# Performance work log

Hardware: AMD Instinct MI355X
Metric: run time of the kernel (lower is better)

Reference implementation:

```python
import jax, jax.numpy as jnp
import numpy as np

# Per-field vocab sizes for the 17 sorted cat fields (ClientID large, ProductID=top1000+UNK)
VOCAB = np.array([500, 50, 100, 3, 1000000, 10, 20, 100, 2, 2, 1001, 4, 4, 50, 2000, 10, 7], dtype=np.int64)
OFFSETS = jnp.asarray(np.concatenate([[0], np.cumsum(VOCAB[:-1])]).astype(np.int32))  # [17]
TOTAL_VOCAB = int(VOCAB.sum())
EMBED_DIM = 16
N_NUM = 23
B = 262144


def setup_inputs() -> dict:
    key = jax.random.key(0)
    k1, k2, k3, k4 = jax.random.split(key, 4)
    # raw randints, folded into each field's valid range
    raw = jax.random.randint(k1, (B, 17), 0, 1000000, dtype=jnp.int32)
    x_cat = raw % jnp.asarray(VOCAB.astype(np.int32))  # [B,17], in-range per field
    x_num = jax.random.normal(k2, (B, N_NUM), dtype=jnp.float32)
    # all 17 per-field embedding tables concatenated into one big table
    table = jax.random.normal(k3, (TOTAL_VOCAB, EMBED_DIM), dtype=jnp.float32) * 0.01
    W_num = jax.random.normal(k4, (EMBED_DIM, N_NUM), dtype=jnp.float32) * 0.1  # Linear(23,16,bias=False) weight
    bias = jnp.zeros((1,), dtype=jnp.float32)  # global_bias
    return {"x_cat": x_cat, "x_num": x_num, "table": table, "W_num": W_num, "bias": bias}


def reference(x_cat, x_num, table, W_num, bias):
    # Fused gather of all 17 field embeddings: E[b,f,:] = embeddings[field_f](x_cat[b,f])
    E = table[x_cat + OFFSETS[None, :]]            # [B,17,16]
    s = E.sum(axis=1)                               # sum of field embeddings, [B,16]
    emb_num = x_num @ W_num.T                       # [B,16]
    # linear_part.sum() in the original
    linear = (s + emb_num).sum(axis=-1)             # [B]
    # sum_{i<j} (e_i . e_j) via 0.5*((sum e)^2 - sum e^2) identity (same math as the double loop)
    inter = 0.5 * ((s * s).sum(axis=-1) - (E * E).sum(axis=(1, 2)))  # [B]
    return bias[0] + linear + inter                 # [B] logits (batched version of scalar logit)
```

## Files before the change

kernel.cpp:

```cpp
#include <hip/hip_runtime.h>

#define NF 17
#define NN 23
#define ED 16
#define BLK 1024
#define RPP 256
#define RPB 512
#define SROWS 862
#define SSTR 20

typedef int   int4u   __attribute__((ext_vector_type(4), aligned(4)));
typedef float float4u __attribute__((ext_vector_type(4), aligned(4)));
typedef float float2u __attribute__((ext_vector_type(2), aligned(4)));

__device__ __forceinline__ void acc4(const float4 v, float& s0, float& s1,
                                     float& s2, float& s3, float& sq) {
    s0 += v.x; s1 += v.y; s2 += v.z; s3 += v.w;
    sq += v.x * v.x + v.y * v.y + v.z * v.z + v.w * v.w;
}

__global__ __launch_bounds__(BLK, 4) void ffm_fwd_kernel(
    const int* __restrict__ x_cat,
    const float* __restrict__ x_num,
    const float* __restrict__ table,
    const float* __restrict__ W_num,
    const float* __restrict__ bias,
    float* __restrict__ out,
    int nrows)
{
    __shared__ float tab[SROWS * SSTR];
    __shared__ float wsum[24];

    const int tid = threadIdx.x;
    const int rl  = tid >> 2;
    const int g   = tid & 3;
    const int wb  = 6 * g;

    const int row0 = blockIdx.x * RPB + rl;
    const int row1 = row0 + RPP;
    const int r0c = (row0 < nrows) ? row0 : (nrows - 1);
    const int r1c = (row1 < nrows) ? row1 : (nrows - 1);

    const int* xc0 = x_cat + (size_t)r0c * NF;
    int4u a0 = *(const int4u*)(xc0);
    int4u a1 = *(const int4u*)(xc0 + 4);
    int4u a2 = *(const int4u*)(xc0 + 8);
    int4u a3 = *(const int4u*)(xc0 + 12);
    int  a16 = xc0[16];
    const float* xp0 = x_num + (size_t)r0c * NN;
    float4u xa0 = *(const float4u*)(xp0 + wb);
    float xb0_0, xb1_0;
    if (g < 3) { const float2u t = *(const float2u*)(xp0 + wb + 4); xb0_0 = t.x; xb1_0 = t.y; }
    else       { xb0_0 = xp0[22]; xb1_0 = 0.f; }

    if (tid < 24) {
        float a = 0.f;
        if (tid < NN) {
            #pragma unroll
            for (int d = 0; d < ED; ++d) a += W_num[d * NN + tid];
        }
        wsum[tid] = a;
    }

    for (int i = tid; i < SROWS * 4; i += BLK) {
        const int r = i >> 2, q = i & 3;
        const int d = (r < 653) ? 0 : (r < 787) ? 1000000 : (r < 845) ? 1001001 : 1003001;
        *(float4*)&tab[r * SSTR + q * 4] =
            *(const float4*)(table + (size_t)(r + d) * ED + q * 4);
    }
    __syncthreads();

    const float b0 = bias[0];
    const float w0 = wsum[wb],     w1 = wsum[wb + 1], w2 = wsum[wb + 2],
                w3 = wsum[wb + 3], w4 = wsum[wb + 4], w5 = wsum[wb + 5];

    const float4 gv00 = *(const float4*)(table + (size_t)(a1.x +     653) * ED + g * 4);
    const float4 gv01 = *(const float4*)(table + (size_t)(a2.z + 1000787) * ED + g * 4);
    const float4 gv02 = *(const float4*)(table + (size_t)(a3.z + 1001846) * ED + g * 4);

    const int* xc1 = x_cat + (size_t)r1c * NF;
    int4u b0v = *(const int4u*)(xc1);
    int4u b1v = *(const int4u*)(xc1 + 4);
    int4u b2v = *(const int4u*)(xc1 + 8);
    int4u b3v = *(const int4u*)(xc1 + 12);
    int  b16v = xc1[16];
    const float* xp1 = x_num + (size_t)r1c * NN;
    float4u xa1 = *(const float4u*)(xp1 + wb);
    float xb0_1, xb1_1;
    if (g < 3) { const float2u t = *(const float2u*)(xp1 + wb + 4); xb0_1 = t.x; xb1_1 = t.y; }
    else       { xb0_1 = xp1[22]; xb1_1 = 0.f; }

    {
        float lin = xa0.x * w0 + xa0.y * w1 + xa0.z * w2 + xa0.w * w3
                  + xb0_0 * w4 + xb1_0 * w5;
        int pr[14];
        pr[0]  = a0.x;        pr[1]  = 500 + a0.y;  pr[2]  = 550 + a0.z;
        pr[3]  = 650 + a0.w;  pr[4]  = 653 + a1.y;  pr[5]  = 663 + a1.z;
        pr[6]  = 683 + a1.w;  pr[7]  = 783 + a2.x;  pr[8]  = 785 + a2.y;
        pr[9]  = 787 + a2.w;  pr[10] = 791 + a3.x;  pr[11] = 795 + a3.y;
        pr[12] = 845 + a3.w;  pr[13] = 855 + a16;

        float s0 = 0.f, s1 = 0.f, s2 = 0.f, s3 = 0.f, sq = 0.f;
        #pragma unroll
        for (int k = 0; k < 14; ++k)
            acc4(*(const float4*)&tab[pr[k] * SSTR + g * 4], s0, s1, s2, s3, sq);

        acc4(gv00, s0, s1, s2, s3, sq);
        acc4(gv01, s0, s1, s2, s3, sq);
        acc4(gv02, s0, s1, s2, s3, sq);

        float ssum = s0 + s1 + s2 + s3;
        float ss2  = s0 * s0 + s1 * s1 + s2 * s2 + s3 * s3;
        #pragma unroll
        for (int m = 1; m <= 2; m <<= 1) {
            ssum += __shfl_xor(ssum, m);
            ss2  += __shfl_xor(ss2, m);
            sq   += __shfl_xor(sq, m);
            lin  += __shfl_xor(lin, m);
        }
        if (g == 0 && row0 < nrows) out[row0] = b0 + ssum + lin + 0.5f * (ss2 - sq);
    }

    const float4 gv10 = *(const float4*)(table + (size_t)(b1v.x +     653) * ED + g * 4);
    const float4 gv11 = *(const float4*)(table + (size_t)(b2v.z + 1000787) * ED + g * 4);
    const float4 gv12 = *(const float4*)(table + (size_t)(b3v.z + 1001846) * ED + g * 4);

    {
        float lin = xa1.x * w0 + xa1.y * w1 + xa1.z * w2 + xa1.w * w3
                  + xb0_1 * w4 + xb1_1 * w5;
        int pr[14];
        pr[0]  = b0v.x;        pr[1]  = 500 + b0v.y;  pr[2]  = 550 + b0v.z;
        pr[3]  = 650 + b0v.w;  pr[4]  = 653 + b1v.y;  pr[5]  = 663 + b1v.z;
        pr[6]  = 683 + b1v.w;  pr[7]  = 783 + b2v.x;  pr[8]  = 785 + b2v.y;
        pr[9]  = 787 + b2v.w;  pr[10] = 791 + b3v.x;  pr[11] = 795 + b3v.y;
        pr[12] = 845 + b3v.w;  pr[13] = 855 + b16v;

        float s0 = 0.f, s1 = 0.f, s2 = 0.f, s3 = 0.f, sq = 0.f;
        #pragma unroll
        for (int k = 0; k < 14; ++k)
            acc4(*(const float4*)&tab[pr[k] * SSTR + g * 4], s0, s1, s2, s3, sq);

        acc4(gv10, s0, s1, s2, s3, sq);
        acc4(gv11, s0, s1, s2, s3, sq);
        acc4(gv12, s0, s1, s2, s3, sq);

        float ssum = s0 + s1 + s2 + s3;
        float ss2  = s0 * s0 + s1 * s1 + s2 * s2 + s3 * s3;
        #pragma unroll
        for (int m = 1; m <= 2; m <<= 1) {
            ssum += __shfl_xor(ssum, m);
            ss2  += __shfl_xor(ss2, m);
            sq   += __shfl_xor(sq, m);
            lin  += __shfl_xor(lin, m);
        }
        if (g == 0 && row1 < nrows) out[row1] = b0 + ssum + lin + 0.5f * (ss2 - sq);
    }
}

extern "C" void kernel_launch(void* const* d_in, const int* in_sizes, int n_in,
                              void* d_out, int out_size, void* d_ws, size_t ws_size,
                              hipStream_t stream) {
    const int*   x_cat = (const int*)  d_in[0];
    const float* x_num = (const float*)d_in[1];
    const float* table = (const float*)d_in[2];
    const float* W_num = (const float*)d_in[3];
    const float* bias  = (const float*)d_in[4];
    float* out = (float*)d_out;

    const int nrows = out_size;
    const int grid = (nrows + RPB - 1) / RPB;
    ffm_fwd_kernel<<<grid, BLK, 0, stream>>>(x_cat, x_num, table, W_num, bias, out, nrows);
}
```

Measured before the change: 21.47 us.

## Issue big-table gathers early, merge shuffle reductions, drop row bounds checks

```diff
diff --git a/kernel.cpp b/kernel.cpp
--- a/kernel.cpp
+++ b/kernel.cpp
@@ -19,7 +19,7 @@
     sq += v.x * v.x + v.y * v.y + v.z * v.z + v.w * v.w;
 }
 
-__global__ __launch_bounds__(BLK, 4) void ffm_fwd_kernel(
+__global__ __launch_bounds__(BLK, 8) void ffm_fwd_kernel(
     const int* __restrict__ x_cat,
     const float* __restrict__ x_num,
     const float* __restrict__ table,
@@ -38,17 +38,19 @@
 
     const int row0 = blockIdx.x * RPB + rl;
     const int row1 = row0 + RPP;
-    const int r0c = (row0 < nrows) ? row0 : (nrows - 1);
-    const int r1c = (row1 < nrows) ? row1 : (nrows - 1);
 
-    const int* xc0 = x_cat + (size_t)r0c * NF;
-    int4u a0 = *(const int4u*)(xc0);
-    int4u a1 = *(const int4u*)(xc0 + 4);
-    int4u a2 = *(const int4u*)(xc0 + 8);
-    int4u a3 = *(const int4u*)(xc0 + 12);
-    int  a16 = xc0[16];
-    const float* xp0 = x_num + (size_t)r0c * NN;
-    float4u xa0 = *(const float4u*)(xp0 + wb);
+    const int* xc0 = x_cat + (size_t)row0 * NF;
+    const int4u a0 = *(const int4u*)(xc0);
+    const int4u a1 = *(const int4u*)(xc0 + 4);
+    const int4u a2 = *(const int4u*)(xc0 + 8);
+    const int4u a3 = *(const int4u*)(xc0 + 12);
+    const int  a16 = xc0[16];
+    const float4 gv00 = *(const float4*)(table + (size_t)(a1.x +     653) * ED + g * 4);
+    const float4 gv01 = *(const float4*)(table + (size_t)(a2.z + 1000787) * ED + g * 4);
+    const float4 gv02 = *(const float4*)(table + (size_t)(a3.z + 1001846) * ED + g * 4);
+
+    const float* xp0 = x_num + (size_t)row0 * NN;
+    const float4u xa0 = *(const float4u*)(xp0 + wb);
     float xb0_0, xb1_0;
     if (g < 3) { const float2u t = *(const float2u*)(xp0 + wb + 4); xb0_0 = t.x; xb1_0 = t.y; }
     else       { xb0_0 = xp0[22]; xb1_0 = 0.f; }
@@ -74,21 +76,12 @@
     const float w0 = wsum[wb],     w1 = wsum[wb + 1], w2 = wsum[wb + 2],
                 w3 = wsum[wb + 3], w4 = wsum[wb + 4], w5 = wsum[wb + 5];
 
-    const float4 gv00 = *(const float4*)(table + (size_t)(a1.x +     653) * ED + g * 4);
-    const float4 gv01 = *(const float4*)(table + (size_t)(a2.z + 1000787) * ED + g * 4);
-    const float4 gv02 = *(const float4*)(table + (size_t)(a3.z + 1001846) * ED + g * 4);
-
-    const int* xc1 = x_cat + (size_t)r1c * NF;
-    int4u b0v = *(const int4u*)(xc1);
-    int4u b1v = *(const int4u*)(xc1 + 4);
-    int4u b2v = *(const int4u*)(xc1 + 8);
-    int4u b3v = *(const int4u*)(xc1 + 12);
-    int  b16v = xc1[16];
-    const float* xp1 = x_num + (size_t)r1c * NN;
-    float4u xa1 = *(const float4u*)(xp1 + wb);
-    float xb0_1, xb1_1;
-    if (g < 3) { const float2u t = *(const float2u*)(xp1 + wb + 4); xb0_1 = t.x; xb1_1 = t.y; }
-    else       { xb0_1 = xp1[22]; xb1_1 = 0.f; }
+    const int* xc1 = x_cat + (size_t)row1 * NF;
+    const int4u c0 = *(const int4u*)(xc1);
+    const int4u c1 = *(const int4u*)(xc1 + 4);
+    const int4u c2 = *(const int4u*)(xc1 + 8);
+    const int4u c3 = *(const int4u*)(xc1 + 12);
+    const int  c16 = xc1[16];
 
     {
         float lin = xa0.x * w0 + xa0.y * w1 + xa0.z * w2 + xa0.w * w3
@@ -109,31 +102,32 @@
         acc4(gv01, s0, s1, s2, s3, sq);
         acc4(gv02, s0, s1, s2, s3, sq);
 
-        float ssum = s0 + s1 + s2 + s3;
-        float ss2  = s0 * s0 + s1 * s1 + s2 * s2 + s3 * s3;
-        #pragma unroll
-        for (int m = 1; m <= 2; m <<= 1) {
-            ssum += __shfl_xor(ssum, m);
-            ss2  += __shfl_xor(ss2, m);
-            sq   += __shfl_xor(sq, m);
-            lin  += __shfl_xor(lin, m);
-        }
-        if (g == 0 && row0 < nrows) out[row0] = b0 + ssum + lin + 0.5f * (ss2 - sq);
+        float contrib = (s0 + s1 + s2 + s3) + lin
+                      + 0.5f * ((s0 * s0 + s1 * s1 + s2 * s2 + s3 * s3) - sq);
+        contrib += __shfl_xor(contrib, 1);
+        contrib += __shfl_xor(contrib, 2);
+        if (g == 0) out[row0] = b0 + contrib;
     }
 
-    const float4 gv10 = *(const float4*)(table + (size_t)(b1v.x +     653) * ED + g * 4);
-    const float4 gv11 = *(const float4*)(table + (size_t)(b2v.z + 1000787) * ED + g * 4);
-    const float4 gv12 = *(const float4*)(table + (size_t)(b3v.z + 1001846) * ED + g * 4);
+    const float4 gv10 = *(const float4*)(table + (size_t)(c1.x +     653) * ED + g * 4);
+    const float4 gv11 = *(const float4*)(table + (size_t)(c2.z + 1000787) * ED + g * 4);
+    const float4 gv12 = *(const float4*)(table + (size_t)(c3.z + 1001846) * ED + g * 4);
+
+    const float* xp1 = x_num + (size_t)row1 * NN;
+    const float4u xa1 = *(const float4u*)(xp1 + wb);
+    float xb0_1, xb1_1;
+    if (g < 3) { const float2u t = *(const float2u*)(xp1 + wb + 4); xb0_1 = t.x; xb1_1 = t.y; }
+    else       { xb0_1 = xp1[22]; xb1_1 = 0.f; }
 
     {
         float lin = xa1.x * w0 + xa1.y * w1 + xa1.z * w2 + xa1.w * w3
                   + xb0_1 * w4 + xb1_1 * w5;
         int pr[14];
-        pr[0]  = b0v.x;        pr[1]  = 500 + b0v.y;  pr[2]  = 550 + b0v.z;
-        pr[3]  = 650 + b0v.w;  pr[4]  = 653 + b1v.y;  pr[5]  = 663 + b1v.z;
-        pr[6]  = 683 + b1v.w;  pr[7]  = 783 + b2v.x;  pr[8]  = 785 + b2v.y;
-        pr[9]  = 787 + b2v.w;  pr[10] = 791 + b3v.x;  pr[11] = 795 + b3v.y;
-        pr[12] = 845 + b3v.w;  pr[13] = 855 + b16v;
+        pr[0]  = c0.x;        pr[1]  = 500 + c0.y;  pr[2]  = 550 + c0.z;
+        pr[3]  = 650 + c0.w;  pr[4]  = 653 + c1.y;  pr[5]  = 663 + c1.z;
+        pr[6]  = 683 + c1.w;  pr[7]  = 783 + c2.x;  pr[8]  = 785 + c2.y;
+        pr[9]  = 787 + c2.w;  pr[10] = 791 + c3.x;  pr[11] = 795 + c3.y;
+        pr[12] = 845 + c3.w;  pr[13] = 855 + c16;
 
         float s0 = 0.f, s1 = 0.f, s2 = 0.f, s3 = 0.f, sq = 0.f;
         #pragma unroll
@@ -144,16 +138,11 @@
         acc4(gv11, s0, s1, s2, s3, sq);
         acc4(gv12, s0, s1, s2, s3, sq);
 
-        float ssum = s0 + s1 + s2 + s3;
-        float ss2  = s0 * s0 + s1 * s1 + s2 * s2 + s3 * s3;
-        #pragma unroll
-        for (int m = 1; m <= 2; m <<= 1) {
-            ssum += __shfl_xor(ssum, m);
-            ss2  += __shfl_xor(ss2, m);
-            sq   += __shfl_xor(sq, m);
-            lin  += __shfl_xor(lin, m);
-        }
-        if (g == 0 && row1 < nrows) out[row1] = b0 + ssum + lin + 0.5f * (ss2 - sq);
+        float contrib = (s0 + s1 + s2 + s3) + lin
+                      + 0.5f * ((s0 * s0 + s1 * s1 + s2 * s2 + s3 * s3) - sq);
+        contrib += __shfl_xor(contrib, 1);
+        contrib += __shfl_xor(contrib, 2);
+        if (g == 0) out[row1] = b0 + contrib;
     }
 }
 
```

New measurement: 19.00 us. -11.5%, faster.
